# Optimization experiments

Hardware: AMD Instinct MI355X
Metric: run time of the kernel (lower is better)

The kernel has to match this reference:

```python
import jax, jax.numpy as jnp
import numpy as np

N, C, E, NUM_ID, NUM_LABELS = 50000, 128, 1600000, 2048, 7


def setup_inputs() -> dict:
    key = jax.random.key(0)
    k_x, k_r, k_c, k_id, k_lab, k_w, k_wid = jax.random.split(key, 7)
    x = jax.random.normal(k_x, (N, C), dtype=jnp.float32)
    row = jax.random.randint(k_r, (E,), 0, N)
    col = jax.random.randint(k_c, (E,), 0, N)
    # remove accidental self-loops so the 'add remaining self loops' step
    # (append all N self loops) matches PyG's add_remaining_self_loops exactly
    col = jnp.where(col == row, (col + 1) % N, col)
    edge_index = jnp.stack([row, col]).astype(jnp.int64)
    idx = jax.random.randint(k_id, (NUM_ID,), 0, N).astype(jnp.int64)
    node_label = jax.random.randint(k_lab, (N,), 0, 8).astype(jnp.int64)
    # glorot init
    s = jnp.sqrt(6.0 / (C + C)).astype(jnp.float32)
    weight = jax.random.uniform(k_w, (C, C), minval=-s, maxval=s, dtype=jnp.float32)
    weight_id = jax.random.uniform(k_wid, (NUM_LABELS, C, C), minval=-s, maxval=s, dtype=jnp.float32)
    return {"x": x, "edge_index": edge_index, "id": idx, "node_label": node_label,
            "weight": weight, "weight_id": weight_id}


def reference(x, edge_index, id, node_label, weight, weight_id):
    n = x.shape[0]
    row, col = edge_index[0], edge_index[1]
    # ego-center update: x[id] += x[id] @ W (index_add handles duplicate ids)
    x = x.at[id].add(x[id] @ weight)
    # label-grouped gather-matmul-scatter: ox = x + sum_i mask_i * (x @ W_i)
    ox = x
    for i in range(NUM_LABELS):
        mask = (node_label == i + 1)
        ox = ox + jnp.where(mask[:, None], x @ weight_id[i], jnp.zeros((), x.dtype))
    # GCN symmetric normalization with self loops (fill_value = 1.0)
    loop = jnp.arange(n)
    row_f = jnp.concatenate([row, loop])
    col_f = jnp.concatenate([col, loop])
    ew = jnp.ones((row_f.shape[0],), dtype=x.dtype)
    deg = jax.ops.segment_sum(ew, row_f, num_segments=n)
    dinv = jnp.where(deg > 0, deg ** -0.5, jnp.zeros((), x.dtype))
    norm = dinv[row_f] * ew * dinv[col_f]
    # message = norm * x_j (source row), aggregated by sum at target col
    out = jax.ops.segment_sum(norm[:, None] * ox[row_f], col_f, num_segments=n)
    return out
```

## Files before the change

kernel.cpp:

```cpp
#include <hip/hip_runtime.h>
#include <hip/hip_bf16.h>

typedef unsigned int   u32;
typedef unsigned short u16;
typedef unsigned char  u8;
typedef float f32x2 __attribute__((ext_vector_type(2)));
typedef float f32x4 __attribute__((ext_vector_type(4)));

#define N_NODES 50000
#define C_DIM   128
#define E_EDGES 1600000
#define NUM_IDX 2048

#define CPB 256
#define NB  196
#define CHK 4096
#define NP  391
#define PT  512
#define GB  8

__global__ void label_hist_kernel(const int* __restrict__ label, int* __restrict__ labCnt,
                                  const int* __restrict__ id, int* __restrict__ cnt) {
    __shared__ int h[8];
    if (threadIdx.x < 8) h[threadIdx.x] = 0;
    __syncthreads();
    int n = blockIdx.x * 256 + threadIdx.x;
    if (n < N_NODES) atomicAdd(&h[label[n]], 1);
    if (n < NUM_IDX) atomicAdd(&cnt[id[n]], 1);
    __syncthreads();
    if (threadIdx.x < 8 && h[threadIdx.x] > 0) atomicAdd(&labCnt[threadIdx.x], h[threadIdx.x]);
}

__global__ void chunk_hist_kernel(const int* __restrict__ row, const int* __restrict__ col,
                                  int* __restrict__ Hc, int* __restrict__ Hr) {
    __shared__ int hc[NB], hr[NB];
    int p = blockIdx.x;
    for (int i = threadIdx.x; i < NB; i += PT) { hc[i] = 0; hr[i] = 0; }
    __syncthreads();
    int e0 = p * CHK, e1 = min(e0 + CHK, E_EDGES);
    for (int e = e0 + threadIdx.x; e < e1; e += PT) {
        atomicAdd(&hc[col[e] >> 8], 1);
        atomicAdd(&hr[row[e] >> 8], 1);
    }
    __syncthreads();
    for (int i = threadIdx.x; i < NB; i += PT) {
        Hc[p * NB + i] = hc[i];
        Hr[p * NB + i] = hr[i];
    }
}

__global__ void offsets_kernel(int* __restrict__ Hc, int* __restrict__ Hr,
                               int* __restrict__ colTot, int* __restrict__ rowTot) {
    __shared__ int sc[PT];
    int b = blockIdx.x;
    int j = (b < NB) ? b : b - NB;
    int* H   = (b < NB) ? Hc : Hr;
    int* tot = (b < NB) ? colTot : rowTot;
    int t = threadIdx.x;
    int v = (t < NP) ? H[t * NB + j] : 0;
    sc[t] = v;
    __syncthreads();
    for (int off = 1; off < PT; off <<= 1) {
        int a = (t >= off) ? sc[t - off] : 0;
        int s = sc[t];
        __syncthreads();
        sc[t] = s + a;
        __syncthreads();
    }
    if (t < NP) H[t * NB + j] = sc[t] - v;
    if (t == PT - 1) tot[j] = sc[t];
}

__global__ void bucket_scan_kernel(const int* __restrict__ colTot, const int* __restrict__ rowTot,
                                   int* __restrict__ bucketStart, int* __restrict__ rowStart,
                                   const int* __restrict__ labCnt, int* __restrict__ labCur) {
    __shared__ int sc[256];
    int t = threadIdx.x;
    sc[t] = (t < NB) ? colTot[t] : 0;
    __syncthreads();
    for (int off = 1; off < 256; off <<= 1) {
        int v = sc[t];
        int a = (t >= off) ? sc[t - off] : 0;
        __syncthreads();
        sc[t] = v + a;
        __syncthreads();
    }
    if (t < NB) {
        bucketStart[t] = (t == 0) ? 0 : sc[t - 1];
        if (t == NB - 1) bucketStart[NB] = sc[t];
    }
    __syncthreads();
    sc[t] = (t < NB) ? rowTot[t] : 0;
    __syncthreads();
    for (int off = 1; off < 256; off <<= 1) {
        int v = sc[t];
        int a = (t >= off) ? sc[t - off] : 0;
        __syncthreads();
        sc[t] = v + a;
        __syncthreads();
    }
    if (t < NB) {
        rowStart[t] = (t == 0) ? 0 : sc[t - 1];
        if (t == NB - 1) rowStart[NB] = sc[t];
    }
    if (t == 0) {
        int run = 0;
        for (int i = 0; i < 8; ++i) { labCur[i] = run; run += labCnt[i]; }
    }
}

__global__ void partition_kernel(const int* __restrict__ row, const int* __restrict__ col,
                                 const int* __restrict__ Hc, const int* __restrict__ Hr,
                                 const int* __restrict__ bucketStart, const int* __restrict__ rowStart,
                                 u32* __restrict__ S, u8* __restrict__ Sr) {
    __shared__ int bc_[NB], br_[NB];
    int p = blockIdx.x;
    for (int i = threadIdx.x; i < NB; i += PT) {
        bc_[i] = bucketStart[i] + Hc[p * NB + i];
        br_[i] = rowStart[i]   + Hr[p * NB + i];
    }
    __syncthreads();
    int e0 = p * CHK, e1 = min(e0 + CHK, E_EDGES);
    for (int e = e0 + threadIdx.x; e < e1; e += PT) {
        int r = row[e], c = col[e];
        int pc = atomicAdd(&bc_[c >> 8], 1);
        S[pc] = ((u32)r << 8) | (u32)(c & 255);
        int pr = atomicAdd(&br_[r >> 8], 1);
        Sr[pr] = (u8)(r & 255);
    }
}

__global__ void label_fill_kernel(const int* __restrict__ label, int* __restrict__ labCur,
                                  int* __restrict__ nodeByLabel) {
    __shared__ int h[8], base[8], c2[8];
    int t = threadIdx.x;
    if (t < 8) { h[t] = 0; c2[t] = 0; }
    __syncthreads();
    int n = blockIdx.x * 256 + t;
    int l = 0;
    if (n < N_NODES) { l = label[n]; atomicAdd(&h[l], 1); }
    __syncthreads();
    if (t < 8 && h[t] > 0) base[t] = atomicAdd(&labCur[t], h[t]);
    __syncthreads();
    if (n < N_NODES) {
        int pos = base[l] + atomicAdd(&c2[l], 1);
        nodeByLabel[pos] = n;
    }
}

__global__ void csr_deg_kernel(const u32* __restrict__ S, const u8* __restrict__ Sr,
                               const int* __restrict__ bucketStart, const int* __restrict__ rowStart,
                               int* __restrict__ start, u16* __restrict__ srcrow,
                               float* __restrict__ dinv) {
    __shared__ int h[CPB], cur[CPB], sc[CPB];
    int t = threadIdx.x;
    if (blockIdx.x >= NB) {
        int b = blockIdx.x - NB;
        if (t < CPB) h[t] = 0;
        __syncthreads();
        int e0 = rowStart[b], e1 = rowStart[b + 1];
        for (int e = e0 + t; e < e1; e += PT) atomicAdd(&h[Sr[e]], 1);
        __syncthreads();
        if (t < CPB) {
            int n = b * CPB + t;
            if (n < N_NODES) dinv[n] = rsqrtf((float)(h[t] + 1));
        }
        return;
    }
    int b = blockIdx.x;
    if (t < CPB) h[t] = 0;
    __syncthreads();
    int e0 = bucketStart[b], e1 = bucketStart[b + 1];
    for (int e = e0 + t; e < e1; e += PT) atomicAdd(&h[S[e] & 255u], 1);
    __syncthreads();
    if (t < CPB) sc[t] = h[t];
    __syncthreads();
    for (int off = 1; off < CPB; off <<= 1) {
        int v = 0, a = 0;
        if (t < CPB) { v = sc[t]; a = (t >= off) ? sc[t - off] : 0; }
        __syncthreads();
        if (t < CPB) sc[t] = v + a;
        __syncthreads();
    }
    if (t < CPB) {
        int base = (t == 0) ? 0 : sc[t - 1];
        int gcol = b * CPB + t;
        if (gcol < N_NODES) start[gcol] = e0 + base;
        cur[t] = base;
    }
    if (b == NB - 1 && t == 0) start[N_NODES] = E_EDGES;
    __syncthreads();
    for (int e = e0 + t; e < e1; e += PT) {
        u32 v = S[e];
        int pos = atomicAdd(&cur[v & 255u], 1);
        srcrow[e0 + pos] = (u16)(v >> 8);
    }
}

__global__ void node_msg_kernel(const float* __restrict__ x,
                                const int* __restrict__ cnt,
                                const int* __restrict__ label,
                                const float* __restrict__ dinv,
                                const float* __restrict__ W,
                                const float* __restrict__ Wid,
                                const int* __restrict__ nodeByLabel,
                                __hip_bfloat16* __restrict__ msgb) {
    __shared__ float xs[GB][C_DIM];
    __shared__ int nid[GB], lab[GB], cc[GB];
    int t = threadIdx.x;
    if (t < GB) {
        int n = nodeByLabel[blockIdx.x * GB + t];
        nid[t] = n; lab[t] = label[n]; cc[t] = cnt[n];
    }
    __syncthreads();
    #pragma unroll
    for (int g = 0; g < GB; ++g)
        xs[g][t] = __builtin_nontemporal_load(x + (size_t)nid[g] * C_DIM + t);
    __syncthreads();
    for (int g = 0; g < GB; ++g) {
        int c = cc[g];
        if (c > 0) {
            float acc = 0.f;
            #pragma unroll 8
            for (int k = 0; k < C_DIM; ++k) acc += xs[g][k] * W[k * C_DIM + t];
            __syncthreads();
            xs[g][t] += (float)c * acc;
            __syncthreads();
        }
    }
    float res[GB];
    #pragma unroll
    for (int g = 0; g < GB; ++g) res[g] = xs[g][t];
    if (lab[0] == lab[GB - 1]) {
        int L = lab[0];
        if (L > 0) {
            const float* Wl = Wid + (size_t)(L - 1) * C_DIM * C_DIM;
            float acc[GB];
            #pragma unroll
            for (int g = 0; g < GB; ++g) acc[g] = 0.f;
            for (int k = 0; k < C_DIM; ++k) {
                float w = Wl[k * C_DIM + t];
                #pragma unroll
                for (int g = 0; g < GB; ++g) acc[g] += xs[g][k] * w;
            }
            #pragma unroll
            for (int g = 0; g < GB; ++g) res[g] += acc[g];
        }
    } else {
        for (int g = 0; g < GB; ++g) {
            int L = lab[g];
            if (L > 0) {
                const float* Wl = Wid + (size_t)(L - 1) * C_DIM * C_DIM;
                float acc = 0.f;
                #pragma unroll 8
                for (int k = 0; k < C_DIM; ++k) acc += xs[g][k] * Wl[k * C_DIM + t];
                res[g] += acc;
            }
        }
    }
    #pragma unroll
    for (int g = 0; g < GB; ++g) {
        int n = nid[g];
        msgb[(size_t)n * C_DIM + t] = __float2bfloat16(dinv[n] * res[g]);
    }
}

__global__ void gather_kernel(const int* __restrict__ start,
                              const u16* __restrict__ srcrow,
                              const float* __restrict__ dinv,
                              const u32* __restrict__ m32,
                              float* __restrict__ out) {
    int wid  = threadIdx.x >> 6;
    int lane = threadIdx.x & 63;
    int g = lane >> 4;
    int q = lane & 15;
    int c = blockIdx.x * 4 + wid;
    int e0 = start[c], e1 = start[c + 1];
    const uint4* m4 = (const uint4*)m32;

    float a0[4], a1[4];
    #pragma unroll
    for (int k = 0; k < 4; ++k) { a0[k] = 0.f; a1[k] = 0.f; }

    #define ACC4(U)                                                          \
        a0[0] += __uint_as_float((U).x << 16); a1[0] += __uint_as_float((U).x & 0xffff0000u); \
        a0[1] += __uint_as_float((U).y << 16); a1[1] += __uint_as_float((U).y & 0xffff0000u); \
        a0[2] += __uint_as_float((U).z << 16); a1[2] += __uint_as_float((U).z & 0xffff0000u); \
        a0[3] += __uint_as_float((U).w << 16); a1[3] += __uint_as_float((U).w & 0xffff0000u);

    int e = e0;
    for (; e + 8 <= e1; e += 8) {
        u32 r0 = srcrow[e + g];
        u32 r1 = srcrow[e + 4 + g];
        uint4 u0 = m4[r0 * 16u + (u32)q];
        uint4 u1 = m4[r1 * 16u + (u32)q];
        ACC4(u0);
        ACC4(u1);
    }
    if (e + 4 <= e1) {
        u32 r0 = srcrow[e + g];
        uint4 u0 = m4[r0 * 16u + (u32)q];
        ACC4(u0);
        e += 4;
    }
    if (g == 0) {
        uint4 us = m4[(u32)c * 16u + (u32)q];
        ACC4(us);
        for (; e < e1; ++e) {
            u32 r = srcrow[e];
            uint4 u = m4[r * 16u + (u32)q];
            ACC4(u);
        }
    }
    #undef ACC4

    #pragma unroll
    for (int k = 0; k < 4; ++k) {
        a0[k] += __shfl_xor(a0[k], 16);
        a0[k] += __shfl_xor(a0[k], 32);
        a1[k] += __shfl_xor(a1[k], 16);
        a1[k] += __shfl_xor(a1[k], 32);
    }

    if (lane < 16) {
        float di = dinv[c];
        f32x4 o0, o1;
        o0.x = di * a0[0]; o0.y = di * a1[0]; o0.z = di * a0[1]; o0.w = di * a1[1];
        o1.x = di * a0[2]; o1.y = di * a1[2]; o1.z = di * a0[3]; o1.w = di * a1[3];
        f32x4* op = (f32x4*)(out + ((size_t)c << 7)) + (q << 1);
        __builtin_nontemporal_store(o0, op);
        __builtin_nontemporal_store(o1, op + 1);
    }
}

extern "C" void kernel_launch(void* const* d_in, const int* in_sizes, int n_in,
                              void* d_out, int out_size, void* d_ws, size_t ws_size,
                              hipStream_t stream) {
    const float* x     = (const float*)d_in[0];
    const int*   edge  = (const int*)d_in[1];
    const int*   id    = (const int*)d_in[2];
    const int*   label = (const int*)d_in[3];
    const float* W     = (const float*)d_in[4];
    const float* Wid   = (const float*)d_in[5];
    float*       out   = (float*)d_out;

    const int* row = edge;
    const int* col = edge + E_EDGES;

    __hip_bfloat16* msgb = (__hip_bfloat16*)d_ws;
    u32* S           = (u32*)(msgb + (size_t)N_NODES * C_DIM);
    u16* srcrow      = (u16*)(S + E_EDGES);
    u8*  Sr          = (u8*)(srcrow + E_EDGES);
    int* start       = (int*)(Sr + E_EDGES);
    int* bucketStart = start + (N_NODES + 1);
    int* rowStart    = bucketStart + (NB + 1);
    int* Hc          = rowStart + (NB + 1);
    int* Hr          = Hc + NP * NB;
    int* colTot      = Hr + NP * NB;
    int* rowTot      = colTot + NB;
    int* nodeByLabel = rowTot + NB;
    float* dinv      = (float*)(nodeByLabel + N_NODES);
    int* cnt         = (int*)(dinv + N_NODES);
    int* labCnt      = cnt + N_NODES;
    int* labCur      = labCnt + 8;

    hipMemsetAsync(cnt, 0, ((size_t)N_NODES + 16) * sizeof(int), stream);

    label_hist_kernel <<<196, 256, 0, stream>>>(label, labCnt, id, cnt);
    chunk_hist_kernel <<<NP, PT, 0, stream>>>(row, col, Hc, Hr);
    offsets_kernel    <<<2 * NB, PT, 0, stream>>>(Hc, Hr, colTot, rowTot);
    bucket_scan_kernel<<<1, 256, 0, stream>>>(colTot, rowTot, bucketStart, rowStart,
                                              labCnt, labCur);
    partition_kernel  <<<NP, PT, 0, stream>>>(row, col, Hc, Hr, bucketStart, rowStart, S, Sr);
    label_fill_kernel <<<196, 256, 0, stream>>>(label, labCur, nodeByLabel);
    csr_deg_kernel    <<<2 * NB, PT, 0, stream>>>(S, Sr, bucketStart, rowStart,
                                                  start, srcrow, dinv);
    node_msg_kernel   <<<N_NODES / GB, C_DIM, 0, stream>>>(x, cnt, label, dinv, W, Wid,
                                                           nodeByLabel, msgb);
    gather_kernel     <<<N_NODES / 4, 256, 0, stream>>>(start, srcrow, dinv,
                                                        (const u32*)msgb, out);
}
```

Measured before the change: 244.4 us.

## Replace prefix-scan bucket partition with fixed-capacity buckets and atomic cursors

```diff
diff --git a/kernel.cpp b/kernel.cpp
--- a/kernel.cpp
+++ b/kernel.cpp
@@ -14,26 +14,40 @@
 
 #define CPB 256
 #define NB  196
+#define CAP 9216
 #define CHK 4096
 #define NP  391
 #define PT  512
 #define GB  8
 
 __global__ void label_hist_kernel(const int* __restrict__ label, int* __restrict__ labCnt,
-                                  const int* __restrict__ id, int* __restrict__ cnt) {
+                                  const int* __restrict__ id, int* __restrict__ cnt,
+                                  int* __restrict__ colCursor, int* __restrict__ rowCursor) {
     __shared__ int h[8];
     if (threadIdx.x < 8) h[threadIdx.x] = 0;
     __syncthreads();
     int n = blockIdx.x * 256 + threadIdx.x;
     if (n < N_NODES) atomicAdd(&h[label[n]], 1);
     if (n < NUM_IDX) atomicAdd(&cnt[id[n]], 1);
+    if (threadIdx.x == 0) {
+        colCursor[blockIdx.x] = blockIdx.x * CAP;
+        rowCursor[blockIdx.x] = blockIdx.x * CAP;
+    }
     __syncthreads();
     if (threadIdx.x < 8 && h[threadIdx.x] > 0) atomicAdd(&labCnt[threadIdx.x], h[threadIdx.x]);
 }
 
-__global__ void chunk_hist_kernel(const int* __restrict__ row, const int* __restrict__ col,
-                                  int* __restrict__ Hc, int* __restrict__ Hr) {
-    __shared__ int hc[NB], hr[NB];
+__global__ void label_base_kernel(const int* __restrict__ labCnt, int* __restrict__ labCur) {
+    if (threadIdx.x == 0) {
+        int run = 0;
+        for (int i = 0; i < 8; ++i) { labCur[i] = run; run += labCnt[i]; }
+    }
+}
+
+__global__ void partition_kernel(const int* __restrict__ row, const int* __restrict__ col,
+                                 int* __restrict__ colCursor, int* __restrict__ rowCursor,
+                                 u32* __restrict__ S, u8* __restrict__ Sr) {
+    __shared__ int hc[NB], hr[NB], bc[NB], br[NB];
     int p = blockIdx.x;
     for (int i = threadIdx.x; i < NB; i += PT) { hc[i] = 0; hr[i] = 0; }
     __syncthreads();
@@ -44,88 +58,15 @@
     }
     __syncthreads();
     for (int i = threadIdx.x; i < NB; i += PT) {
-        Hc[p * NB + i] = hc[i];
-        Hr[p * NB + i] = hr[i];
-    }
-}
-
-__global__ void offsets_kernel(int* __restrict__ Hc, int* __restrict__ Hr,
-                               int* __restrict__ colTot, int* __restrict__ rowTot) {
-    __shared__ int sc[PT];
-    int b = blockIdx.x;
-    int j = (b < NB) ? b : b - NB;
-    int* H   = (b < NB) ? Hc : Hr;
-    int* tot = (b < NB) ? colTot : rowTot;
-    int t = threadIdx.x;
-    int v = (t < NP) ? H[t * NB + j] : 0;
-    sc[t] = v;
-    __syncthreads();
-    for (int off = 1; off < PT; off <<= 1) {
-        int a = (t >= off) ? sc[t - off] : 0;
-        int s = sc[t];
-        __syncthreads();
-        sc[t] = s + a;
-        __syncthreads();
-    }
-    if (t < NP) H[t * NB + j] = sc[t] - v;
-    if (t == PT - 1) tot[j] = sc[t];
-}
-
-__global__ void bucket_scan_kernel(const int* __restrict__ colTot, const int* __restrict__ rowTot,
-                                   int* __restrict__ bucketStart, int* __restrict__ rowStart,
-                                   const int* __restrict__ labCnt, int* __restrict__ labCur) {
-    __shared__ int sc[256];
-    int t = threadIdx.x;
-    sc[t] = (t < NB) ? colTot[t] : 0;
-    __syncthreads();
-    for (int off = 1; off < 256; off <<= 1) {
-        int v = sc[t];
-        int a = (t >= off) ? sc[t - off] : 0;
-        __syncthreads();
-        sc[t] = v + a;
-        __syncthreads();
-    }
-    if (t < NB) {
-        bucketStart[t] = (t == 0) ? 0 : sc[t - 1];
-        if (t == NB - 1) bucketStart[NB] = sc[t];
-    }
-    __syncthreads();
-    sc[t] = (t < NB) ? rowTot[t] : 0;
-    __syncthreads();
-    for (int off = 1; off < 256; off <<= 1) {
-        int v = sc[t];
-        int a = (t >= off) ? sc[t - off] : 0;
-        __syncthreads();
-        sc[t] = v + a;
-        __syncthreads();
-    }
-    if (t < NB) {
-        rowStart[t] = (t == 0) ? 0 : sc[t - 1];
-        if (t == NB - 1) rowStart[NB] = sc[t];
-    }
-    if (t == 0) {
-        int run = 0;
-        for (int i = 0; i < 8; ++i) { labCur[i] = run; run += labCnt[i]; }
-    }
-}
-
-__global__ void partition_kernel(const int* __restrict__ row, const int* __restrict__ col,
-                                 const int* __restrict__ Hc, const int* __restrict__ Hr,
-                                 const int* __restrict__ bucketStart, const int* __restrict__ rowStart,
-                                 u32* __restrict__ S, u8* __restrict__ Sr) {
-    __shared__ int bc_[NB], br_[NB];
-    int p = blockIdx.x;
-    for (int i = threadIdx.x; i < NB; i += PT) {
-        bc_[i] = bucketStart[i] + Hc[p * NB + i];
-        br_[i] = rowStart[i]   + Hr[p * NB + i];
-    }
-    __syncthreads();
-    int e0 = p * CHK, e1 = min(e0 + CHK, E_EDGES);
+        bc[i] = (hc[i] > 0) ? atomicAdd(&colCursor[i], hc[i]) : 0;
+        br[i] = (hr[i] > 0) ? atomicAdd(&rowCursor[i], hr[i]) : 0;
+    }
+    __syncthreads();
     for (int e = e0 + threadIdx.x; e < e1; e += PT) {
         int r = row[e], c = col[e];
-        int pc = atomicAdd(&bc_[c >> 8], 1);
+        int pc = atomicAdd(&bc[c >> 8], 1);
         S[pc] = ((u32)r << 8) | (u32)(c & 255);
-        int pr = atomicAdd(&br_[r >> 8], 1);
+        int pr = atomicAdd(&br[r >> 8], 1);
         Sr[pr] = (u8)(r & 255);
     }
 }
@@ -149,16 +90,16 @@
 }
 
 __global__ void csr_deg_kernel(const u32* __restrict__ S, const u8* __restrict__ Sr,
-                               const int* __restrict__ bucketStart, const int* __restrict__ rowStart,
-                               int* __restrict__ start, u16* __restrict__ srcrow,
-                               float* __restrict__ dinv) {
+                               const int* __restrict__ colCursor, const int* __restrict__ rowCursor,
+                               int* __restrict__ s_beg, int* __restrict__ s_end,
+                               u16* __restrict__ srcrow, float* __restrict__ dinv) {
     __shared__ int h[CPB], cur[CPB], sc[CPB];
     int t = threadIdx.x;
     if (blockIdx.x >= NB) {
         int b = blockIdx.x - NB;
         if (t < CPB) h[t] = 0;
         __syncthreads();
-        int e0 = rowStart[b], e1 = rowStart[b + 1];
+        int e0 = b * CAP, e1 = rowCursor[b];
         for (int e = e0 + t; e < e1; e += PT) atomicAdd(&h[Sr[e]], 1);
         __syncthreads();
         if (t < CPB) {
@@ -170,7 +111,7 @@
     int b = blockIdx.x;
     if (t < CPB) h[t] = 0;
     __syncthreads();
-    int e0 = bucketStart[b], e1 = bucketStart[b + 1];
+    int e0 = b * CAP, e1 = colCursor[b];
     for (int e = e0 + t; e < e1; e += PT) atomicAdd(&h[S[e] & 255u], 1);
     __syncthreads();
     if (t < CPB) sc[t] = h[t];
@@ -185,10 +126,12 @@
     if (t < CPB) {
         int base = (t == 0) ? 0 : sc[t - 1];
         int gcol = b * CPB + t;
-        if (gcol < N_NODES) start[gcol] = e0 + base;
+        if (gcol < N_NODES) {
+            s_beg[gcol] = e0 + base;
+            s_end[gcol] = e0 + base + h[t];
+        }
         cur[t] = base;
     }
-    if (b == NB - 1 && t == 0) start[N_NODES] = E_EDGES;
     __syncthreads();
     for (int e = e0 + t; e < e1; e += PT) {
         u32 v = S[e];
@@ -265,7 +208,7 @@
     }
 }
 
-__global__ void gather_kernel(const int* __restrict__ start,
+__global__ void gather_kernel(const int* __restrict__ s_beg, const int* __restrict__ s_end,
                               const u16* __restrict__ srcrow,
                               const float* __restrict__ dinv,
                               const u32* __restrict__ m32,
@@ -275,7 +218,7 @@
     int g = lane >> 4;
     int q = lane & 15;
     int c = blockIdx.x * 4 + wid;
-    int e0 = start[c], e1 = start[c + 1];
+    int e0 = s_beg[c], e1 = s_end[c];
     const uint4* m4 = (const uint4*)m32;
 
     float a0[4], a1[4];
@@ -349,16 +292,13 @@
 
     __hip_bfloat16* msgb = (__hip_bfloat16*)d_ws;
     u32* S           = (u32*)(msgb + (size_t)N_NODES * C_DIM);
-    u16* srcrow      = (u16*)(S + E_EDGES);
-    u8*  Sr          = (u8*)(srcrow + E_EDGES);
-    int* start       = (int*)(Sr + E_EDGES);
-    int* bucketStart = start + (N_NODES + 1);
-    int* rowStart    = bucketStart + (NB + 1);
-    int* Hc          = rowStart + (NB + 1);
-    int* Hr          = Hc + NP * NB;
-    int* colTot      = Hr + NP * NB;
-    int* rowTot      = colTot + NB;
-    int* nodeByLabel = rowTot + NB;
+    u16* srcrow      = (u16*)(S + (size_t)NB * CAP);
+    u8*  Sr          = (u8*)(srcrow + (size_t)NB * CAP);
+    int* s_beg       = (int*)(Sr + (size_t)NB * CAP);
+    int* s_end       = s_beg + N_NODES;
+    int* colCursor   = s_end + N_NODES;
+    int* rowCursor   = colCursor + NB;
+    int* nodeByLabel = rowCursor + NB;
     float* dinv      = (float*)(nodeByLabel + N_NODES);
     int* cnt         = (int*)(dinv + N_NODES);
     int* labCnt      = cnt + N_NODES;
@@ -366,17 +306,14 @@
 
     hipMemsetAsync(cnt, 0, ((size_t)N_NODES + 16) * sizeof(int), stream);
 
-    label_hist_kernel <<<196, 256, 0, stream>>>(label, labCnt, id, cnt);
-    chunk_hist_kernel <<<NP, PT, 0, stream>>>(row, col, Hc, Hr);
-    offsets_kernel    <<<2 * NB, PT, 0, stream>>>(Hc, Hr, colTot, rowTot);
-    bucket_scan_kernel<<<1, 256, 0, stream>>>(colTot, rowTot, bucketStart, rowStart,
-                                              labCnt, labCur);
-    partition_kernel  <<<NP, PT, 0, stream>>>(row, col, Hc, Hr, bucketStart, rowStart, S, Sr);
+    label_hist_kernel <<<196, 256, 0, stream>>>(label, labCnt, id, cnt, colCursor, rowCursor);
+    label_base_kernel <<<1, 64, 0, stream>>>(labCnt, labCur);
+    partition_kernel  <<<NP, PT, 0, stream>>>(row, col, colCursor, rowCursor, S, Sr);
     label_fill_kernel <<<196, 256, 0, stream>>>(label, labCur, nodeByLabel);
-    csr_deg_kernel    <<<2 * NB, PT, 0, stream>>>(S, Sr, bucketStart, rowStart,
-                                                  start, srcrow, dinv);
+    csr_deg_kernel    <<<2 * NB, PT, 0, stream>>>(S, Sr, colCursor, rowCursor,
+                                                  s_beg, s_end, srcrow, dinv);
     node_msg_kernel   <<<N_NODES / GB, C_DIM, 0, stream>>>(x, cnt, label, dinv, W, Wid,
                                                            nodeByLabel, msgb);
-    gather_kernel     <<<N_NODES / 4, 256, 0, stream>>>(start, srcrow, dinv,
+    gather_kernel     <<<N_NODES / 4, 256, 0, stream>>>(s_beg, s_end, srcrow, dinv,
                                                         (const u32*)msgb, out);
 }
```

Result: faster. 237.2 us (-2.9%).
